# Optimization experiments

Measured on AMD Instinct MI355X. Metric: run time of the kernel, lower is better.

## Reference

```python
import jax, jax.numpy as jnp
import numpy as np

B, T, D, H = 4096, 1024, 3, 64


def setup_inputs() -> dict:
    key = jax.random.key(0)
    ks = jax.random.split(key, 10)
    s_ih = 1.0 / np.sqrt(H)
    return {
        "x1": jax.random.normal(ks[0], (B, T, D), dtype=jnp.float32),
        "x2": jax.random.normal(ks[1], (B, T, D), dtype=jnp.float32),
        # PyTorch nn.GRU params, gate order (r, z, n)
        "W_ih": jax.random.uniform(ks[2], (3 * H, D), jnp.float32, -s_ih, s_ih),
        "W_hh": jax.random.uniform(ks[3], (3 * H, H), jnp.float32, -s_ih, s_ih),
        "b_ih": jax.random.uniform(ks[4], (3 * H,), jnp.float32, -s_ih, s_ih),
        "b_hh": jax.random.uniform(ks[5], (3 * H,), jnp.float32, -s_ih, s_ih),
        # MLP head: Linear(64,32) -> ReLU -> Linear(32,1) -> Sigmoid
        "W1": jax.random.uniform(ks[6], (32, H), jnp.float32, -s_ih, s_ih),
        "b1": jax.random.uniform(ks[7], (32,), jnp.float32, -s_ih, s_ih),
        "W2": jax.random.uniform(ks[8], (1, 32), jnp.float32, -1 / np.sqrt(32), 1 / np.sqrt(32)),
        "b2": jax.random.uniform(ks[9], (1,), jnp.float32, -1 / np.sqrt(32), 1 / np.sqrt(32)),
    }


def _gru_last_hidden(x, W_ih, W_hh, b_ih, b_hh):
    # x: [B, T, D] -> final hidden state [B, H], PyTorch GRU semantics.
    xs = jnp.swapaxes(x, 0, 1)  # [T, B, D]

    def step(h, xt):
        xg = xt @ W_ih.T + b_ih            # [B, 3H]
        hg = h @ W_hh.T + b_hh             # [B, 3H]
        xr, xz, xn = jnp.split(xg, 3, axis=-1)
        hr, hz, hn = jnp.split(hg, 3, axis=-1)
        r = jax.nn.sigmoid(xr + hr)
        z = jax.nn.sigmoid(xz + hz)
        n = jnp.tanh(xn + r * hn)
        h_new = (1.0 - z) * n + z * h
        return h_new, None

    h0 = jnp.zeros((x.shape[0], W_hh.shape[1]), dtype=x.dtype)
    h_last, _ = jax.lax.scan(step, h0, xs)
    return h_last


def reference(x1, x2, W_ih, W_hh, b_ih, b_hh, W1, b1, W2, b2):
    h1 = _gru_last_hidden(x1, W_ih, W_hh, b_ih, b_hh)
    h2 = _gru_last_hidden(x2, W_ih, W_hh, b_ih, b_hh)
    diff = jnp.abs(h1 - h2)                                # [B, H]
    hid = jax.nn.relu(diff @ W1.T + b1)                    # [B, 32]
    out = jax.nn.sigmoid(hid @ W2.T + b2)                  # [B, 1]
    return out
```

## Files before the change

### kernel.cpp

```cpp
#include <hip/hip_runtime.h>
#include <math.h>

#define T_ 1024
#define D_ 3
#define H_ 64

typedef _Float16 f16x8 __attribute__((ext_vector_type(8)));
typedef float f32x4 __attribute__((ext_vector_type(4)));

__device__ __forceinline__ float sigmoid_f(float x) {
    return __builtin_amdgcn_rcpf(1.0f + __expf(-x));
}

#define MFMA(A, B, C) __builtin_amdgcn_mfma_f32_16x16x32_f16((A), (B), (C), 0, 0, 0)

#define LDS_BARRIER() asm volatile("s_waitcnt lgkmcnt(0)\ns_barrier" ::: "memory")

__global__ __launch_bounds__(256, 2) void gru_mfma9(
    const float* __restrict__ x1, const float* __restrict__ x2,
    const float* __restrict__ W_ih, const float* __restrict__ W_hh,
    const float* __restrict__ b_ih, const float* __restrict__ b_hh,
    const float* __restrict__ W1, const float* __restrict__ b1,
    const float* __restrict__ W2, const float* __restrict__ b2,
    float* __restrict__ out)
{
    const int lane = threadIdx.x & 63;
    const int w    = threadIdx.x >> 6;
    const int c    = lane & 15;
    const int q    = lane >> 4;
    const int u    = 16 * w + c;
    const int seq0 = blockIdx.x * 8;

    const float SRZ = -1.44269504f;
    const float SN  =  2.88539008f;
    const float gsc[3] = {SRZ, SRZ, SN};

    f16x8 wf[3][2];
    #pragma unroll
    for (int g = 0; g < 3; ++g)
        #pragma unroll
        for (int ks = 0; ks < 2; ++ks) {
            const float* p = W_hh + (size_t)(g * 64 + u) * H_ + 32 * ks + q * 8;
            f16x8 v;
            #pragma unroll
            for (int j = 0; j < 8; ++j) v[j] = (_Float16)(p[j] * gsc[g]);
            wf[g][ks] = v;
        }

    f16x8 bxf[3];
    #pragma unroll
    for (int g = 0; g < 3; ++g) {
        f16x8 v = {};
        if (q == 0) {
            #pragma unroll
            for (int d = 0; d < 3; ++d)
                v[d] = (_Float16)(W_ih[(size_t)(g * 64 + u) * D_ + d] * gsc[g]);
        }
        bxf[g] = v;
    }

    const float comb_r = (b_ih[u]      + b_hh[u])      * SRZ;
    const float comb_z = (b_ih[64 + u] + b_hh[64 + u]) * SRZ;
    const float bxn    = b_ih[128 + u] * SN;
    const float bhn    = b_hh[128 + u] * SN;
    const f32x4 Cr  = {comb_r, comb_r, comb_r, comb_r};
    const f32x4 Cz  = {comb_z, comb_z, comb_z, comb_z};
    const f32x4 Cxn = {bxn, bxn, bxn, bxn};
    const f32x4 Chn = {bhn, bhn, bhn, bhn};

    const float* xptr = (c < 8) ? (x1 + (size_t)(seq0 + c) * (T_ * D_))
                                : (x2 + (size_t)(seq0 + c - 8) * (T_ * D_));

    __shared__ alignas(16) _Float16 hb[2][16 * 72];
    __shared__ float dlds[8][68];

    float h[4];
    #pragma unroll
    for (int r = 0; r < 4; ++r) h[r] = 0.f;

    auto step = [&](int buf, float x0, float x1v, float x2v) {
        #pragma unroll
        for (int r = 0; r < 4; ++r)
            hb[buf][(4 * q + r) * 72 + u] = (_Float16)h[r];
        f16x8 ax = {};
        ax[0] = (_Float16)x0; ax[1] = (_Float16)x1v; ax[2] = (_Float16)x2v;
        f32x4 ar  = MFMA(ax, bxf[0], Cr);
        f32x4 az  = MFMA(ax, bxf[1], Cz);
        f32x4 axn = MFMA(ax, bxf[2], Cxn);
        LDS_BARRIER();
        const f16x8 a0 = *(const f16x8*)&hb[buf][c * 72 + q * 8];
        const f16x8 a1 = *(const f16x8*)&hb[buf][c * 72 + 32 + q * 8];

        ar = MFMA(a0, wf[0][0], ar);
        az = MFMA(a0, wf[1][0], az);
        ar = MFMA(a1, wf[0][1], ar);
        az = MFMA(a1, wf[1][1], az);
        f32x4 ahn = MFMA(a0, wf[2][0], Chn);
        ahn = MFMA(a1, wf[2][1], ahn);

        #pragma unroll
        for (int r = 0; r < 4; ++r) {
            const float eu = __builtin_amdgcn_exp2f(ar[r]);
            const float ev = __builtin_amdgcn_exp2f(az[r]);
            const float pu = 1.0f + eu, pv = 1.0f + ev;
            const float inv = __builtin_amdgcn_rcpf(pu * pv);
            const float rr = pv * inv;
            const float zz = pu * inv;
            const float tt = axn[r] + rr * ahn[r];
            const float e2 = __builtin_amdgcn_exp2f(tt);
            const float nn = 1.0f - 2.0f * __builtin_amdgcn_rcpf(e2 + 1.0f);
            h[r] = nn + zz * (h[r] - nn);
        }
    };

    const float4* xp4 = (const float4*)xptr;
    float4 xc[3];
    #pragma unroll
    for (int i = 0; i < 3; ++i) xc[i] = xp4[i];

    for (int t = 0; t < T_; t += 4) {
        float4 xn[3];
        const int tb = (t + 4 < T_) ? (3 * (t + 4)) / 4 : (3 * t) / 4;
        #pragma unroll
        for (int i = 0; i < 3; ++i) xn[i] = xp4[tb + i];
        step(0, xc[0].x, xc[0].y, xc[0].z);
        step(1, xc[0].w, xc[1].x, xc[1].y);
        step(0, xc[1].z, xc[1].w, xc[2].x);
        step(1, xc[2].y, xc[2].z, xc[2].w);
        #pragma unroll
        for (int i = 0; i < 3; ++i) xc[i] = xn[i];
    }

    #pragma unroll
    for (int r = 0; r < 4; ++r) {
        const float o = __shfl_xor(h[r], 32);
        if (q < 2) dlds[4 * q + r][u] = fabsf(h[r] - o);
    }
    __syncthreads();
    if (w == 0) {
        const int s = lane >> 3;
        const int b = lane & 7;
        float am[4];
        #pragma unroll
        for (int i = 0; i < 4; ++i) am[i] = b1[b + 8 * i];
        #pragma unroll
        for (int k4 = 0; k4 < 16; ++k4) {
            const float4 dvec = *(const float4*)&dlds[s][k4 * 4];
            #pragma unroll
            for (int i = 0; i < 4; ++i) {
                const float4 wv = *(const float4*)&W1[(b + 8 * i) * H_ + k4 * 4];
                am[i] += dvec.x * wv.x + dvec.y * wv.y + dvec.z * wv.z + dvec.w * wv.w;
            }
        }
        float part = 0.f;
        #pragma unroll
        for (int i = 0; i < 4; ++i) part += fmaxf(am[i], 0.f) * W2[b + 8 * i];
        part += __shfl_xor(part, 1);
        part += __shfl_xor(part, 2);
        part += __shfl_xor(part, 4);
        if (b == 0) out[seq0 + s] = sigmoid_f(part + b2[0]);
    }
}

extern "C" void kernel_launch(void* const* d_in, const int* in_sizes, int n_in,
                              void* d_out, int out_size, void* d_ws, size_t ws_size,
                              hipStream_t stream) {
    const float* x1   = (const float*)d_in[0];
    const float* x2   = (const float*)d_in[1];
    const float* W_ih = (const float*)d_in[2];
    const float* W_hh = (const float*)d_in[3];
    const float* b_ih = (const float*)d_in[4];
    const float* b_hh = (const float*)d_in[5];
    const float* W1   = (const float*)d_in[6];
    const float* b1   = (const float*)d_in[7];
    const float* W2   = (const float*)d_in[8];
    const float* b2   = (const float*)d_in[9];

    const int B = in_sizes[0] / (T_ * D_);
    dim3 grid(B / 8), block(256);
    gru_mfma9<<<grid, block, 0, stream>>>(x1, x2, W_ih, W_hh, b_ih, b_hh,
                                          W1, b1, W2, b2, (float*)d_out);
}
```

Measured before the change: 584.8 us.

## Interleave two independent GRU batches per block to hide barrier and MFMA latency

Each block now processes 16 sequences as two 16-row MFMA tiles (x1 batch and x2 batch) whose recurrence phases are interleaved. While one tile waits on its LDS barrier, the other tile's MFMAs and gate math run, hiding dependency latency within one workgroup. The grid is halved and launch bounds relaxed to one block per CU-slot, which trades inter-block overlap for intra-block overlap and raises register use. The final diff is computed directly from the paired registers instead of through a lane shuffle.

```diff
diff --git a/kernel.cpp b/kernel.cpp
--- a/kernel.cpp
+++ b/kernel.cpp
@@ -13,10 +13,9 @@
 }
 
 #define MFMA(A, B, C) __builtin_amdgcn_mfma_f32_16x16x32_f16((A), (B), (C), 0, 0, 0)
-
 #define LDS_BARRIER() asm volatile("s_waitcnt lgkmcnt(0)\ns_barrier" ::: "memory")
 
-__global__ __launch_bounds__(256, 2) void gru_mfma9(
+__global__ __launch_bounds__(256, 1) void gru_dualphase(
     const float* __restrict__ x1, const float* __restrict__ x2,
     const float* __restrict__ W_ih, const float* __restrict__ W_hh,
     const float* __restrict__ b_ih, const float* __restrict__ b_hh,
@@ -29,7 +28,7 @@
     const int c    = lane & 15;
     const int q    = lane >> 4;
     const int u    = 16 * w + c;
-    const int seq0 = blockIdx.x * 8;
+    const int seq0 = blockIdx.x * 16;
 
     const float SRZ = -1.44269504f;
     const float SN  =  2.88539008f;
@@ -68,36 +67,32 @@
     const f32x4 Cxn = {bxn, bxn, bxn, bxn};
     const f32x4 Chn = {bhn, bhn, bhn, bhn};
 
-    const float* xptr = (c < 8) ? (x1 + (size_t)(seq0 + c) * (T_ * D_))
-                                : (x2 + (size_t)(seq0 + c - 8) * (T_ * D_));
-
-    __shared__ alignas(16) _Float16 hb[2][16 * 72];
-    __shared__ float dlds[8][68];
-
-    float h[4];
-    #pragma unroll
-    for (int r = 0; r < 4; ++r) h[r] = 0.f;
-
-    auto step = [&](int buf, float x0, float x1v, float x2v) {
-        #pragma unroll
-        for (int r = 0; r < 4; ++r)
-            hb[buf][(4 * q + r) * 72 + u] = (_Float16)h[r];
+    const float4* xpA = (const float4*)(x1 + (size_t)(seq0 + c) * (T_ * D_));
+    const float4* xpB = (const float4*)(x2 + (size_t)(seq0 + c) * (T_ * D_));
+
+    __shared__ alignas(16) _Float16 hbA[16 * 72];
+    __shared__ alignas(16) _Float16 hbB[16 * 72];
+    __shared__ float dlds[16][68];
+
+    float hA[4], hB[4];
+    #pragma unroll
+    for (int r = 0; r < 4; ++r) { hA[r] = 0.f; hB[r] = 0.f; }
+
+    f32x4 arA, azA, axnA;
+    f32x4 arB, azB, axnB;
+    f16x8 fa0, fa1;
+
+    auto xprep = [&](float x0, float x1v, float x2v,
+                     f32x4& ar, f32x4& az, f32x4& axn) {
         f16x8 ax = {};
         ax[0] = (_Float16)x0; ax[1] = (_Float16)x1v; ax[2] = (_Float16)x2v;
-        f32x4 ar  = MFMA(ax, bxf[0], Cr);
-        f32x4 az  = MFMA(ax, bxf[1], Cz);
-        f32x4 axn = MFMA(ax, bxf[2], Cxn);
-        LDS_BARRIER();
-        const f16x8 a0 = *(const f16x8*)&hb[buf][c * 72 + q * 8];
-        const f16x8 a1 = *(const f16x8*)&hb[buf][c * 72 + 32 + q * 8];
-
-        ar = MFMA(a0, wf[0][0], ar);
-        az = MFMA(a0, wf[1][0], az);
-        ar = MFMA(a1, wf[0][1], ar);
-        az = MFMA(a1, wf[1][1], az);
-        f32x4 ahn = MFMA(a0, wf[2][0], Chn);
-        ahn = MFMA(a1, wf[2][1], ahn);
-
+        ar  = MFMA(ax, bxf[0], Cr);
+        az  = MFMA(ax, bxf[1], Cz);
+        axn = MFMA(ax, bxf[2], Cxn);
+    };
+
+    auto gates = [&](const f32x4& ar, const f32x4& az, const f32x4& axn,
+                     const f32x4& ahn, float (&h)[4]) {
         #pragma unroll
         for (int r = 0; r < 4; ++r) {
             const float eu = __builtin_amdgcn_exp2f(ar[r]);
@@ -113,32 +108,72 @@
         }
     };
 
-    const float4* xp4 = (const float4*)xptr;
-    float4 xc[3];
-    #pragma unroll
-    for (int i = 0; i < 3; ++i) xc[i] = xp4[i];
-
-    for (int t = 0; t < T_; t += 4) {
-        float4 xn[3];
-        const int tb = (t + 4 < T_) ? (3 * (t + 4)) / 4 : (3 * t) / 4;
-        #pragma unroll
-        for (int i = 0; i < 3; ++i) xn[i] = xp4[tb + i];
-        step(0, xc[0].x, xc[0].y, xc[0].z);
-        step(1, xc[0].w, xc[1].x, xc[1].y);
-        step(0, xc[1].z, xc[1].w, xc[2].x);
-        step(1, xc[2].y, xc[2].z, xc[2].w);
-        #pragma unroll
-        for (int i = 0; i < 3; ++i) xc[i] = xn[i];
-    }
+    float4 xcA[3], xcB[3];
+    #pragma unroll
+    for (int i = 0; i < 3; ++i) { xcA[i] = xpA[i]; xcB[i] = xpB[i]; }
 
     #pragma unroll
     for (int r = 0; r < 4; ++r) {
-        const float o = __shfl_xor(h[r], 32);
-        if (q < 2) dlds[4 * q + r][u] = fabsf(h[r] - o);
-    }
+        hbA[(4 * q + r) * 72 + u] = (_Float16)0.f;
+        hbB[(4 * q + r) * 72 + u] = (_Float16)0.f;
+    }
+    xprep(xcA[0].x, xcA[0].y, xcA[0].z, arA, azA, axnA);
+    xprep(xcB[0].x, xcB[0].y, xcB[0].z, arB, azB, axnB);
+    LDS_BARRIER();
+    fa0 = *(const f16x8*)&hbA[c * 72 + q * 8];
+    fa1 = *(const f16x8*)&hbA[c * 72 + 32 + q * 8];
+
+    auto iter = [&](float a0x, float a1x, float a2x,
+                    float b0x, float b1x, float b2x) {
+        arA = MFMA(fa0, wf[0][0], arA);
+        azA = MFMA(fa0, wf[1][0], azA);
+        f32x4 ahnA = MFMA(fa0, wf[2][0], Chn);
+        arA = MFMA(fa1, wf[0][1], arA);
+        azA = MFMA(fa1, wf[1][1], azA);
+        ahnA = MFMA(fa1, wf[2][1], ahnA);
+        gates(arA, azA, axnA, ahnA, hA);
+        LDS_BARRIER();
+        const f16x8 fb0 = *(const f16x8*)&hbB[c * 72 + q * 8];
+        const f16x8 fb1 = *(const f16x8*)&hbB[c * 72 + 32 + q * 8];
+        #pragma unroll
+        for (int r = 0; r < 4; ++r)
+            hbA[(4 * q + r) * 72 + u] = (_Float16)hA[r];
+        xprep(a0x, a1x, a2x, arA, azA, axnA);
+        arB = MFMA(fb0, wf[0][0], arB);
+        azB = MFMA(fb0, wf[1][0], azB);
+        f32x4 ahnB = MFMA(fb0, wf[2][0], Chn);
+        arB = MFMA(fb1, wf[0][1], arB);
+        azB = MFMA(fb1, wf[1][1], azB);
+        ahnB = MFMA(fb1, wf[2][1], ahnB);
+        gates(arB, azB, axnB, ahnB, hB);
+        LDS_BARRIER();
+        fa0 = *(const f16x8*)&hbA[c * 72 + q * 8];
+        fa1 = *(const f16x8*)&hbA[c * 72 + 32 + q * 8];
+        #pragma unroll
+        for (int r = 0; r < 4; ++r)
+            hbB[(4 * q + r) * 72 + u] = (_Float16)hB[r];
+        xprep(b0x, b1x, b2x, arB, azB, axnB);
+    };
+
+    for (int t0 = 0; t0 < T_; t0 += 4) {
+        float4 xnA[3], xnB[3];
+        const int tb = (t0 + 4 < T_) ? (3 * (t0 + 4)) / 4 : (3 * t0) / 4;
+        #pragma unroll
+        for (int i = 0; i < 3; ++i) { xnA[i] = xpA[tb + i]; xnB[i] = xpB[tb + i]; }
+        iter(xcA[0].w, xcA[1].x, xcA[1].y, xcB[0].w, xcB[1].x, xcB[1].y);
+        iter(xcA[1].z, xcA[1].w, xcA[2].x, xcB[1].z, xcB[1].w, xcB[2].x);
+        iter(xcA[2].y, xcA[2].z, xcA[2].w, xcB[2].y, xcB[2].z, xcB[2].w);
+        iter(xnA[0].x, xnA[0].y, xnA[0].z, xnB[0].x, xnB[0].y, xnB[0].z);
+        #pragma unroll
+        for (int i = 0; i < 3; ++i) { xcA[i] = xnA[i]; xcB[i] = xnB[i]; }
+    }
+
+    #pragma unroll
+    for (int r = 0; r < 4; ++r)
+        dlds[4 * q + r][u] = fabsf(hA[r] - hB[r]);
     __syncthreads();
-    if (w == 0) {
-        const int s = lane >> 3;
+    if (w < 2) {
+        const int s = 8 * w + (lane >> 3);
         const int b = lane & 7;
         float am[4];
         #pragma unroll
@@ -177,7 +212,7 @@
     const float* b2   = (const float*)d_in[9];
 
     const int B = in_sizes[0] / (T_ * D_);
-    dim3 grid(B / 8), block(256);
-    gru_mfma9<<<grid, block, 0, stream>>>(x1, x2, W_ih, W_hh, b_ih, b_hh,
-                                          W1, b1, W2, b2, (float*)d_out);
+    dim3 grid(B / 16), block(256);
+    gru_dualphase<<<grid, block, 0, stream>>>(x1, x2, W_ih, W_hh, b_ih, b_hh,
+                                              W1, b1, W2, b2, (float*)d_out);
 }
```

New measurement: 868.2 us. 48.5% more time.
